# Kernel tuning notes

Measured on AMD Instinct MI355X. Metric: run time of the kernel, lower is better.

The kernel has to match this reference:

```python
import jax, jax.numpy as jnp
import numpy as np

IN_F, OUT_F, BLOCK, NBLK = 1024, 4096, 256, 16
TOPK = NBLK // 4  # 4, as in forward: n_blocks // 4


def setup_inputs() -> dict:
    key = jax.random.key(0)
    ks = jax.random.split(key, 7)
    s = 1.0 / np.sqrt(IN_F)
    s2 = 1.0 / np.sqrt(OUT_F)
    return {
        "x": jax.random.normal(ks[0], (4, 4096, IN_F), jnp.float32),
        "router_w": jax.random.uniform(ks[1], (NBLK, IN_F), jnp.float32, -s, s),
        "router_b": jax.random.uniform(ks[2], (NBLK,), jnp.float32, -s, s),
        "w1": jax.random.uniform(ks[3], (OUT_F, IN_F), jnp.float32, -s, s),
        "b1": jax.random.uniform(ks[4], (OUT_F,), jnp.float32, -s, s),
        "w2": jax.random.uniform(ks[5], (IN_F, OUT_F), jnp.float32, -s2, s2),
        "b2": jax.random.uniform(ks[6], (IN_F,), jnp.float32, -s2, s2),
    }


def reference(x, router_w, router_b, w1, b1, w2, b2):
    x_shape = x.shape
    xf = x.reshape(-1, IN_F)  # [N, d]
    n = xf.shape[0]
    # router: Linear + softmax, then top-k block selection per token
    prob = jax.nn.softmax(xf @ router_w.T + router_b, axis=-1)  # [N, n_blocks]
    _, idx = jax.lax.top_k(prob, TOPK)  # [N, k]
    mask = jnp.zeros((n, NBLK), bool).at[jnp.arange(n)[:, None], idx].set(True)
    # RoutedLinearRow: per-block fc1, zeros at unselected blocks
    w1b = w1.reshape(NBLK, BLOCK, IN_F)
    b1b = b1.reshape(NBLK, BLOCK)
    h = jnp.einsum('nd,ibd->nib', xf, w1b) + b1b  # [N, n_blocks, block]
    h = jnp.where(mask[:, :, None], h, jnp.zeros((), h.dtype))
    h = jax.nn.relu(h)
    # RoutedLinearCol: only selected blocks contribute
    w2b = w2.reshape(IN_F, NBLK, BLOCK)
    y = jnp.einsum('nib,dib->nd', jnp.where(mask[:, :, None], h, 0.0), w2b) + b2
    return y.reshape(x_shape)
```

## Files before the change

kernel.cpp:

```cpp
#include <hip/hip_runtime.h>
#include <hip/hip_bf16.h>

#define NTOK   16384
#define INF    1024
#define OUTF   4096
#define NBLK   16
#define BLKSZ  256
#define KTOP   4

typedef short bf16x8 __attribute__((ext_vector_type(8)));
typedef float f32x4 __attribute__((ext_vector_type(4)));
typedef unsigned short u16x8 __attribute__((ext_vector_type(8)));

__device__ __forceinline__ unsigned short f2bf(float f) {
  unsigned u = __float_as_uint(f);
  u += 0x7FFFu + ((u >> 16) & 1u);
  return (unsigned short)(u >> 16);
}

__device__ __forceinline__ void load_lds16(const void* g, void* l) {
  __builtin_amdgcn_global_load_lds(
      (const __attribute__((address_space(1))) unsigned int*)g,
      (__attribute__((address_space(3))) unsigned int*)l, 16, 0, 0);
}

__device__ __forceinline__ double shfl_xor_d(double v, int m) {
  long long l = __double_as_longlong(v);
  int lo = (int)(l & 0xFFFFFFFFll), hi = (int)(l >> 32);
  lo = __shfl_xor(lo, m);
  hi = __shfl_xor(hi, m);
  return __longlong_as_double(((long long)hi << 32) | (unsigned long long)(unsigned)lo);
}

__device__ __forceinline__ int pi_perm(int j) {
  return (j & 128) | ((j & 7) << 4) | ((j >> 3) & 15);
}

__global__ __launch_bounds__(256) void k_cvt_router(
    const float* __restrict__ x, const float* __restrict__ rw,
    const float* __restrict__ rb, const float* __restrict__ w1,
    const float* __restrict__ w2, const float* __restrict__ b1,
    unsigned* __restrict__ tok_blocks, unsigned* __restrict__ counts,
    unsigned short* __restrict__ xb, unsigned short* __restrict__ w1b,
    unsigned short* __restrict__ w2p, float* __restrict__ b1p) {
  __shared__ float4 rwl[4096];
  const int tid = threadIdx.x;
  const float4* rw4 = (const float4*)rw;
  for (int i = tid; i < 4096; i += 256) rwl[i] = rw4[i];
  __syncthreads();

  const int n = blockIdx.x * 32 + (tid >> 3);
  const int q = tid & 7;
  double p[16];
#pragma unroll
  for (int j = 0; j < 16; ++j) p[j] = 0.0;
  const float4* xr = (const float4*)(x + (size_t)n * INF);
  ushort4* xbr = (ushort4*)(xb + (size_t)n * INF);
#pragma unroll 4
  for (int i = 0; i < 32; ++i) {
    const int d4 = q + i * 8;
    const float4 xv = xr[d4];
    ushort4 o;
    o.x = f2bf(xv.x); o.y = f2bf(xv.y); o.z = f2bf(xv.z); o.w = f2bf(xv.w);
    xbr[d4] = o;
#pragma unroll
    for (int j = 0; j < 16; ++j) {
      const float4 wv = rwl[j * 256 + d4];
      p[j] = fma((double)xv.x, (double)wv.x, p[j]);
      p[j] = fma((double)xv.y, (double)wv.y, p[j]);
      p[j] = fma((double)xv.z, (double)wv.z, p[j]);
      p[j] = fma((double)xv.w, (double)wv.w, p[j]);
    }
  }
#pragma unroll
  for (int j = 0; j < 16; ++j) {
    double v = p[j];
    v += shfl_xor_d(v, 1);
    v += shfl_xor_d(v, 2);
    v += shfl_xor_d(v, 4);
    p[j] = v + (double)rb[j];
  }

  __syncthreads();
  unsigned* hist = (unsigned*)rwl;
  if (tid < 16) hist[tid] = 0;
  __syncthreads();

  if (q == 0) {
    unsigned packed = 0;
#pragma unroll
    for (int j = 0; j < 16; ++j) {
      int r = 0;
#pragma unroll
      for (int j2 = 0; j2 < 16; ++j2)
        r += (int)((p[j2] > p[j]) | ((p[j2] == p[j]) & (j2 < j)));
      if (r < KTOP) packed |= (unsigned)j << (8 * r);
    }
    tok_blocks[n] = packed;
    atomicAdd(&hist[packed & 15u], 1u);
    atomicAdd(&hist[(packed >> 8) & 15u], 1u);
    atomicAdd(&hist[(packed >> 16) & 15u], 1u);
    atomicAdd(&hist[(packed >> 24) & 15u], 1u);
  }
  __syncthreads();
  if (tid < 16 && hist[tid]) atomicAdd(&counts[tid], hist[tid]);

  const size_t stride = (size_t)gridDim.x * 256;
  for (size_t i = (size_t)blockIdx.x * 256 + tid; i < 1573376; i += stride) {
    if (i < 1048576) {
      float4 v = ((const float4*)w1)[i];
      ushort4 o;
      o.x = f2bf(v.x); o.y = f2bf(v.y); o.z = f2bf(v.z); o.w = f2bf(v.w);
      ((ushort4*)w1b)[i] = o;
    } else if (i < 1572864) {
      const size_t g = i - 1048576;
      const int d = (int)(g >> 9);
      const int rest = (int)(g & 511);
      const int jg = rest * 8;
      const int blk = jg >> 8;
      const int j0 = jg & 255;
      const float* src = w2 + (size_t)d * 4096 + blk * 256;
      u16x8 o;
#pragma unroll
      for (int ni = 0; ni < 8; ++ni) o[ni] = f2bf(src[pi_perm(j0 + ni)]);
      *(u16x8*)(w2p + (size_t)d * 4096 + jg) = o;
    } else {
      const int idx = (int)(i - 1572864);
      const int jg = idx * 8;
      const int blk = jg >> 8;
      const int j0 = jg & 255;
      const float* src = b1 + blk * 256;
      float o[8];
#pragma unroll
      for (int ni = 0; ni < 8; ++ni) o[ni] = src[pi_perm(j0 + ni)];
      float4* dst = (float4*)(b1p + jg);
      dst[0] = make_float4(o[0], o[1], o[2], o[3]);
      dst[1] = make_float4(o[4], o[5], o[6], o[7]);
    }
  }
}

__global__ __launch_bounds__(256) void k_build(
    const unsigned* __restrict__ tok_blocks, const unsigned* __restrict__ counts,
    unsigned* __restrict__ alloc, unsigned short* __restrict__ list) {
  unsigned offl[16];
  {
    unsigned o = 0;
#pragma unroll
    for (int i = 0; i < 16; ++i) { offl[i] = o; o += (counts[i] + 127u) & ~127u; }
  }
  const int n = blockIdx.x * 256 + threadIdx.x;
  const unsigned packed = tok_blocks[n];
  const int lane = threadIdx.x & 63;
#pragma unroll
  for (int b = 0; b < 16; ++b) {
    int r = -1;
#pragma unroll
    for (int q = 0; q < 4; ++q)
      if (((packed >> (8 * q)) & 15u) == (unsigned)b) r = q;
    unsigned long long m = __ballot(r >= 0);
    if (m) {
      int leader = __ffsll((unsigned long long)m) - 1;
      unsigned base = 0;
      if (lane == leader) base = offl[b] + atomicAdd(&alloc[b], (unsigned)__popcll(m));
      base = (unsigned)__shfl((int)base, leader);
      if (r >= 0) {
        unsigned pos = base + (unsigned)__popcll(m & ((1ull << lane) - 1ull));
        list[pos] = (unsigned short)(n | (r << 14));
      }
    }
  }
}

__global__ __launch_bounds__(256, 2) void k_ffn(
    const unsigned short* __restrict__ xb, const unsigned short* __restrict__ w1b,
    const unsigned short* __restrict__ w2p, const float* __restrict__ b1p,
    const unsigned short* __restrict__ list, const unsigned* __restrict__ counts,
    unsigned short* __restrict__ part) {
  __shared__ __align__(16) char lds[73728];
  char* const As0 = lds + 32768;
  char* const As1 = lds + 36864;
  char* const Bs0 = lds + 40960;
  char* const Bs1 = lds + 57344;

  const int bid0 = blockIdx.x;
  const int bid = (bid0 & 7) * 256 + (bid0 >> 3);
  const int blk = bid >> 7;
  const int tile = bid & 127;
  unsigned cnt = 0, goffBase = 0;
  {
    unsigned o = 0;
#pragma unroll
    for (int i = 0; i < 16; ++i) {
      const unsigned c = counts[i];
      if (i == blk) { cnt = c; goffBase = o; }
      o += (c + 127u) & ~127u;
    }
  }
  if ((unsigned)(tile * 64) >= cnt) return;
  const unsigned goff = goffBase + tile * 64;
  const int rem = (int)cnt - tile * 64;

  const int tid = threadIdx.x;
  const int lane = tid & 63;
  const int wid = tid >> 6;
  const int wr = wid >> 1;
  const int wc = wid & 1;
  const int c16 = lane & 15;
  const int kc = lane >> 4;

  const int srow = tid >> 2;
  const int schunk = tid & 3;
  const unsigned tokS = list[goff + srow] & 0x3FFFu;

#define STAGE_A(buf, k0)                                                        \
  load_lds16(xb + (size_t)tokS * INF + (k0) +                                   \
                 ((schunk ^ ((srow >> 1) & 3)) * 8),                            \
             (buf) + tid * 16);

#define STAGE_B1(buf, k0)                                                       \
  _Pragma("unroll")                                                             \
  for (int l = 0; l < 4; ++l) {                                                 \
    const int idx = l * 256 + tid;                                              \
    const int row = idx >> 2;                                                   \
    load_lds16(w1b + (size_t)(blk * 256 + row) * INF + (k0) +                   \
                   (((idx & 3) ^ ((row >> 1) & 3)) * 8),                        \
               (buf) + idx * 16);                                               \
  }

#define COMPUTE_A(abuf, bbuf)                                                   \
  {                                                                             \
    bf16x8 a[2], b[8];                                                          \
    _Pragma("unroll")                                                           \
    for (int mi = 0; mi < 2; ++mi) {                                            \
      const int row = wr * 32 + mi * 16 + c16;                                  \
      a[mi] = *(const bf16x8*)((abuf) + row * 64 +                              \
                               ((kc ^ ((row >> 1) & 3)) << 4));                 \
    }                                                                           \
    _Pragma("unroll")                                                           \
    for (int ni = 0; ni < 8; ++ni) {                                            \
      const int row = wc * 128 + ni * 16 + c16;                                 \
      b[ni] = *(const bf16x8*)((bbuf) + row * 64 +                              \
                               ((kc ^ ((row >> 1) & 3)) << 4));                 \
    }                                                                           \
    _Pragma("unroll")                                                           \
    for (int mi = 0; mi < 2; ++mi)                                              \
      _Pragma("unroll")                                                         \
      for (int ni = 0; ni < 8; ++ni)                                            \
        acc[mi][ni] =                                                           \
            __builtin_amdgcn_mfma_f32_16x16x32_bf16(a[mi], b[ni], acc[mi][ni], 0, 0, 0); \
  }

  f32x4 acc[2][8] = {};
  STAGE_A(As0, 0);
  STAGE_B1(Bs0, 0);
  __syncthreads();
#pragma unroll 1
  for (int kk = 0; kk < 16; ++kk) {
    const int k0 = kk * 64;
    STAGE_A(As1, k0 + 32);
    STAGE_B1(Bs1, k0 + 32);
    COMPUTE_A(As0, Bs0);
    __syncthreads();
    if (kk < 15) {
      STAGE_A(As0, k0 + 64);
      STAGE_B1(Bs0, k0 + 64);
    }
    COMPUTE_A(As1, Bs1);
    __syncthreads();
  }

#define STAGE_B2(buf, it)                                                       \
  {                                                                             \
    const int ns2 = (it) >> 3, k02 = ((it) & 7) * 32;                           \
    _Pragma("unroll")                                                           \
    for (int l = 0; l < 4; ++l) {                                               \
      const int idx = l * 256 + tid;                                            \
      const int row = idx >> 2;                                                 \
      load_lds16(w2p + (size_t)(ns2 * 256 + row) * OUTF + blk * 256 + k02 +     \
                     (((idx & 3) ^ ((row >> 1) & 3)) * 8),                      \
                 (buf) + idx * 16);                                             \
    }                                                                           \
  }

#define COMPUTE_B(bbuf, k02)                                                    \
  {                                                                             \
    bf16x8 a[2], b[8];                                                          \
    _Pragma("unroll")                                                           \
    for (int mi = 0; mi < 2; ++mi) {                                            \
      const int row = wr * 32 + mi * 16 + c16;                                  \
      const int co = ((k02) >> 3) + kc;                                         \
      a[mi] = *(const bf16x8*)(lds + row * 512 +                                \
                               (((co & ~7) | ((co & 7) ^ (row & 7))) << 4));    \
    }                                                                           \
    _Pragma("unroll")                                                           \
    for (int ni = 0; ni < 8; ++ni) {                                            \
      const int row = wc * 128 + ni * 16 + c16;                                 \
      b[ni] = *(const bf16x8*)((bbuf) + row * 64 +                              \
                               ((kc ^ ((row >> 1) & 3)) << 4));                 \
    }                                                                           \
    _Pragma("unroll")                                                           \
    for (int mi = 0; mi < 2; ++mi)                                              \
      _Pragma("unroll")                                                         \
      for (int ni = 0; ni < 8; ++ni)                                            \
        acc2[mi][ni] =                                                          \
            __builtin_amdgcn_mfma_f32_16x16x32_bf16(a[mi], b[ni], acc2[mi][ni], 0, 0, 0); \
  }

  STAGE_B2(Bs0, 0);

  {
    const float4* bp = (const float4*)(b1p + blk * 256 + wc * 128 + c16 * 8);
    const float4 bv0 = bp[0], bv1 = bp[1];
    const float bvv[8] = {bv0.x, bv0.y, bv0.z, bv0.w, bv1.x, bv1.y, bv1.z, bv1.w};
    const int chunk = wc * 16 + c16;
    const int cslot = (chunk & ~7);
    const int clow  = (chunk & 7);
#pragma unroll
    for (int mi = 0; mi < 2; ++mi) {
#pragma unroll
      for (int i = 0; i < 4; ++i) {
        const int row = wr * 32 + mi * 16 + (lane >> 4) * 4 + i;
        u16x8 wv;
#pragma unroll
        for (int ni = 0; ni < 8; ++ni) {
          float v = acc[mi][ni][i] + bvv[ni];
          v = v > 0.f ? v : 0.f;
          wv[ni] = f2bf(v);
        }
        *(u16x8*)(lds + row * 512 + ((cslot | (clow ^ (row & 7))) << 4)) = wv;
      }
    }
  }
  __syncthreads();

#pragma unroll 1
  for (int ns = 0; ns < 4; ++ns) {
    f32x4 acc2[2][8] = {};
#pragma unroll 1
    for (int jj = 0; jj < 4; ++jj) {
      const int it = ns * 8 + jj * 2;
      STAGE_B2(Bs1, it + 1);
      COMPUTE_B(Bs0, jj * 64);
      __syncthreads();
      if (it + 2 < 32) STAGE_B2(Bs0, it + 2);
      COMPUTE_B(Bs1, jj * 64 + 32);
      __syncthreads();
    }
#pragma unroll
    for (int mi = 0; mi < 2; ++mi) {
#pragma unroll
      for (int i = 0; i < 4; ++i) {
        const int row = wr * 32 + mi * 16 + (lane >> 4) * 4 + i;
        if (row < rem) {
          const unsigned e = list[goff + row];
          u16x8 wv;
#pragma unroll
          for (int ni = 0; ni < 8; ++ni) wv[ni] = f2bf(acc2[mi][ni][i]);
          *(u16x8*)(part + ((size_t)(e & 0x3FFFu) * 4 + (e >> 14)) * 1024 +
                    ns * 256 + wc * 128 + c16 * 8) = wv;
        }
      }
    }
  }
#undef STAGE_A
#undef STAGE_B1
#undef STAGE_B2
#undef COMPUTE_A
#undef COMPUTE_B
}

__global__ __launch_bounds__(256) void k_reduce(const unsigned short* __restrict__ part,
                                                const float* __restrict__ b2,
                                                float* __restrict__ out) {
  __shared__ float lds[8 * 1028];
  const int tid = threadIdx.x;
  const int tok0 = blockIdx.x * 8;
  const int tok_l = tid >> 5;
  const int l32 = tid & 31;
  const unsigned short* pbase = part + (size_t)(tok0 + tok_l) * 4096;

#pragma unroll
  for (int g = 0; g < 4; ++g) {
    const int idx = g * 32 + l32;
    const int p0 = idx * 8;
    float s[8] = {0.f, 0.f, 0.f, 0.f, 0.f, 0.f, 0.f, 0.f};
#pragma unroll
    for (int sl = 0; sl < 4; ++sl) {
      u16x8 v = *(const u16x8*)(pbase + sl * 1024 + p0);
#pragma unroll
      for (int j = 0; j < 8; ++j)
        s[j] += __uint_as_float((unsigned)(unsigned short)v[j] << 16);
    }
    const int ns = idx >> 5, wcb = (idx >> 4) & 1, cc = idx & 15;
#pragma unroll
    for (int ni = 0; ni < 8; ++ni)
      lds[tok_l * 1028 + ns * 256 + wcb * 128 + ni * 16 + cc] = s[ni];
  }
  __syncthreads();
  const float4 b2v = ((const float4*)b2)[tid];
#pragma unroll
  for (int r = 0; r < 8; ++r) {
    f32x4 lv = *(f32x4*)&lds[r * 1028 + tid * 4];
    float4 o = make_float4(lv[0] + b2v.x, lv[1] + b2v.y, lv[2] + b2v.z, lv[3] + b2v.w);
    *(float4*)(out + (size_t)(tok0 + r) * 1024 + tid * 4) = o;
  }
}

extern "C" void kernel_launch(void* const* d_in, const int* in_sizes, int n_in,
                              void* d_out, int out_size, void* d_ws, size_t ws_size,
                              hipStream_t stream) {
  const float* x  = (const float*)d_in[0];
  const float* rw = (const float*)d_in[1];
  const float* rb = (const float*)d_in[2];
  const float* w1 = (const float*)d_in[3];
  const float* b1 = (const float*)d_in[4];
  const float* w2 = (const float*)d_in[5];
  const float* b2 = (const float*)d_in[6];
  float* out = (float*)d_out;

  char* ws = (char*)d_ws;
  unsigned short* part = (unsigned short*)(ws);
  unsigned short* xb   = (unsigned short*)(ws + 134217728);
  unsigned short* w1b  = (unsigned short*)(ws + 167772160);
  unsigned short* w2p  = (unsigned short*)(ws + 176160768);
  unsigned* tokb       = (unsigned*)(ws + 184549376);
  unsigned short* list = (unsigned short*)(ws + 184614912);
  float* b1p           = (float*)(ws + 184750080);
  unsigned* counts     = (unsigned*)(ws + 184766464);
  unsigned* alloc      = (unsigned*)(ws + 184766528);

  hipMemsetAsync(ws + 184766464, 0, 128, stream);
  k_cvt_router<<<dim3(512), dim3(256), 0, stream>>>(x, rw, rb, w1, w2, b1, tokb,
                                                    counts, xb, w1b, w2p, b1p);
  k_build<<<dim3(64), dim3(256), 0, stream>>>(tokb, counts, alloc, list);
  k_ffn<<<dim3(2048), dim3(256), 0, stream>>>(xb, w1b, w2p, b1p, list, counts, part);
  k_reduce<<<dim3(2048), dim3(256), 0, stream>>>(part, b2, out);
}
```

Before: 287.1 us.

## Split FFN tile across 8 waves with narrower per-wave N slices

```diff
diff --git a/kernel.cpp b/kernel.cpp
--- a/kernel.cpp
+++ b/kernel.cpp
@@ -11,6 +11,7 @@
 typedef short bf16x8 __attribute__((ext_vector_type(8)));
 typedef float f32x4 __attribute__((ext_vector_type(4)));
 typedef unsigned short u16x8 __attribute__((ext_vector_type(8)));
+typedef unsigned short u16x4 __attribute__((ext_vector_type(4)));
 
 __device__ __forceinline__ unsigned short f2bf(float f) {
   unsigned u = __float_as_uint(f);
@@ -32,8 +33,8 @@
   return __longlong_as_double(((long long)hi << 32) | (unsigned long long)(unsigned)lo);
 }
 
-__device__ __forceinline__ int pi_perm(int j) {
-  return (j & 128) | ((j & 7) << 4) | ((j >> 3) & 15);
+__device__ __forceinline__ int pi2(int j) {
+  return (j & 192) | ((j & 3) << 4) | ((j >> 2) & 15);
 }
 
 __global__ __launch_bounds__(256) void k_cvt_router(
@@ -122,7 +123,7 @@
       const float* src = w2 + (size_t)d * 4096 + blk * 256;
       u16x8 o;
 #pragma unroll
-      for (int ni = 0; ni < 8; ++ni) o[ni] = f2bf(src[pi_perm(j0 + ni)]);
+      for (int ni = 0; ni < 8; ++ni) o[ni] = f2bf(src[pi2(j0 + ni)]);
       *(u16x8*)(w2p + (size_t)d * 4096 + jg) = o;
     } else {
       const int idx = (int)(i - 1572864);
@@ -132,7 +133,7 @@
       const float* src = b1 + blk * 256;
       float o[8];
 #pragma unroll
-      for (int ni = 0; ni < 8; ++ni) o[ni] = src[pi_perm(j0 + ni)];
+      for (int ni = 0; ni < 8; ++ni) o[ni] = src[pi2(j0 + ni)];
       float4* dst = (float4*)(b1p + jg);
       dst[0] = make_float4(o[0], o[1], o[2], o[3]);
       dst[1] = make_float4(o[4], o[5], o[6], o[7]);
@@ -172,7 +173,7 @@
   }
 }
 
-__global__ __launch_bounds__(256, 2) void k_ffn(
+__global__ __launch_bounds__(512, 4) void k_ffn(
     const unsigned short* __restrict__ xb, const unsigned short* __restrict__ w1b,
     const unsigned short* __restrict__ w2p, const float* __restrict__ b1p,
     const unsigned short* __restrict__ list, const unsigned* __restrict__ counts,
@@ -204,24 +205,25 @@
   const int tid = threadIdx.x;
   const int lane = tid & 63;
   const int wid = tid >> 6;
-  const int wr = wid >> 1;
-  const int wc = wid & 1;
+  const int wr = wid >> 2;
+  const int wc = wid & 3;
   const int c16 = lane & 15;
-  const int kc = lane >> 4;
+  const int kc4 = lane >> 4;
 
   const int srow = tid >> 2;
   const int schunk = tid & 3;
-  const unsigned tokS = list[goff + srow] & 0x3FFFu;
+  const unsigned tokS = list[goff + (srow & 63)] & 0x3FFFu;
 
 #define STAGE_A(buf, k0)                                                        \
-  load_lds16(xb + (size_t)tokS * INF + (k0) +                                   \
-                 ((schunk ^ ((srow >> 1) & 3)) * 8),                            \
-             (buf) + tid * 16);
+  if (tid < 256)                                                                \
+    load_lds16(xb + (size_t)tokS * INF + (k0) +                                 \
+                   ((schunk ^ ((srow >> 1) & 3)) * 8),                          \
+               (buf) + tid * 16);
 
 #define STAGE_B1(buf, k0)                                                       \
   _Pragma("unroll")                                                             \
-  for (int l = 0; l < 4; ++l) {                                                 \
-    const int idx = l * 256 + tid;                                              \
+  for (int l = 0; l < 2; ++l) {                                                 \
+    const int idx = l * 512 + tid;                                              \
     const int row = idx >> 2;                                                   \
     load_lds16(w1b + (size_t)(blk * 256 + row) * INF + (k0) +                   \
                    (((idx & 3) ^ ((row >> 1) & 3)) * 8),                        \
@@ -230,28 +232,28 @@
 
 #define COMPUTE_A(abuf, bbuf)                                                   \
   {                                                                             \
-    bf16x8 a[2], b[8];                                                          \
+    bf16x8 a[2], b[4];                                                          \
     _Pragma("unroll")                                                           \
     for (int mi = 0; mi < 2; ++mi) {                                            \
       const int row = wr * 32 + mi * 16 + c16;                                  \
       a[mi] = *(const bf16x8*)((abuf) + row * 64 +                              \
-                               ((kc ^ ((row >> 1) & 3)) << 4));                 \
+                               ((kc4 ^ ((row >> 1) & 3)) << 4));                \
     }                                                                           \
     _Pragma("unroll")                                                           \
-    for (int ni = 0; ni < 8; ++ni) {                                            \
-      const int row = wc * 128 + ni * 16 + c16;                                 \
+    for (int ni = 0; ni < 4; ++ni) {                                            \
+      const int row = wc * 64 + ni * 16 + c16;                                  \
       b[ni] = *(const bf16x8*)((bbuf) + row * 64 +                              \
-                               ((kc ^ ((row >> 1) & 3)) << 4));                 \
+                               ((kc4 ^ ((row >> 1) & 3)) << 4));                \
     }                                                                           \
     _Pragma("unroll")                                                           \
     for (int mi = 0; mi < 2; ++mi)                                              \
       _Pragma("unroll")                                                         \
-      for (int ni = 0; ni < 8; ++ni)                                            \
+      for (int ni = 0; ni < 4; ++ni)                                            \
         acc[mi][ni] =                                                           \
             __builtin_amdgcn_mfma_f32_16x16x32_bf16(a[mi], b[ni], acc[mi][ni], 0, 0, 0); \
   }
 
-  f32x4 acc[2][8] = {};
+  f32x4 acc[2][4] = {};
   STAGE_A(As0, 0);
   STAGE_B1(Bs0, 0);
   __syncthreads();
@@ -274,8 +276,8 @@
   {                                                                             \
     const int ns2 = (it) >> 3, k02 = ((it) & 7) * 32;                           \
     _Pragma("unroll")                                                           \
-    for (int l = 0; l < 4; ++l) {                                               \
-      const int idx = l * 256 + tid;                                            \
+    for (int l = 0; l < 2; ++l) {                                               \
+      const int idx = l * 512 + tid;                                            \
       const int row = idx >> 2;                                                 \
       load_lds16(w2p + (size_t)(ns2 * 256 + row) * OUTF + blk * 256 + k02 +     \
                      (((idx & 3) ^ ((row >> 1) & 3)) * 8),                      \
@@ -285,24 +287,24 @@
 
 #define COMPUTE_B(bbuf, k02)                                                    \
   {                                                                             \
-    bf16x8 a[2], b[8];                                                          \
+    bf16x8 a[2], b[4];                                                          \
     _Pragma("unroll")                                                           \
     for (int mi = 0; mi < 2; ++mi) {                                            \
       const int row = wr * 32 + mi * 16 + c16;                                  \
-      const int co = ((k02) >> 3) + kc;                                         \
+      const int co = ((k02) >> 3) + kc4;                                        \
       a[mi] = *(const bf16x8*)(lds + row * 512 +                                \
                                (((co & ~7) | ((co & 7) ^ (row & 7))) << 4));    \
     }                                                                           \
     _Pragma("unroll")                                                           \
-    for (int ni = 0; ni < 8; ++ni) {                                            \
-      const int row = wc * 128 + ni * 16 + c16;                                 \
+    for (int ni = 0; ni < 4; ++ni) {                                            \
+      const int row = wc * 64 + ni * 16 + c16;                                  \
       b[ni] = *(const bf16x8*)((bbuf) + row * 64 +                              \
-                               ((kc ^ ((row >> 1) & 3)) << 4));                 \
+                               ((kc4 ^ ((row >> 1) & 3)) << 4));                \
     }                                                                           \
     _Pragma("unroll")                                                           \
     for (int mi = 0; mi < 2; ++mi)                                              \
       _Pragma("unroll")                                                         \
-      for (int ni = 0; ni < 8; ++ni)                                            \
+      for (int ni = 0; ni < 4; ++ni)                                            \
         acc2[mi][ni] =                                                          \
             __builtin_amdgcn_mfma_f32_16x16x32_bf16(a[mi], b[ni], acc2[mi][ni], 0, 0, 0); \
   }
@@ -310,25 +312,22 @@
   STAGE_B2(Bs0, 0);
 
   {
-    const float4* bp = (const float4*)(b1p + blk * 256 + wc * 128 + c16 * 8);
-    const float4 bv0 = bp[0], bv1 = bp[1];
-    const float bvv[8] = {bv0.x, bv0.y, bv0.z, bv0.w, bv1.x, bv1.y, bv1.z, bv1.w};
-    const int chunk = wc * 16 + c16;
-    const int cslot = (chunk & ~7);
-    const int clow  = (chunk & 7);
+    const float4 bv = *(const float4*)(b1p + blk * 256 + wc * 64 + c16 * 4);
+    const float bvv[4] = {bv.x, bv.y, bv.z, bv.w};
 #pragma unroll
     for (int mi = 0; mi < 2; ++mi) {
 #pragma unroll
       for (int i = 0; i < 4; ++i) {
         const int row = wr * 32 + mi * 16 + (lane >> 4) * 4 + i;
-        u16x8 wv;
-#pragma unroll
-        for (int ni = 0; ni < 8; ++ni) {
+        u16x4 wv;
+#pragma unroll
+        for (int ni = 0; ni < 4; ++ni) {
           float v = acc[mi][ni][i] + bvv[ni];
           v = v > 0.f ? v : 0.f;
           wv[ni] = f2bf(v);
         }
-        *(u16x8*)(lds + row * 512 + ((cslot | (clow ^ (row & 7))) << 4)) = wv;
+        *(u16x4*)(lds + row * 512 +
+                  ((wc * 8 + ((c16 >> 1) ^ (row & 7))) << 4) + (c16 & 1) * 8) = wv;
       }
     }
   }
@@ -336,7 +335,7 @@
 
 #pragma unroll 1
   for (int ns = 0; ns < 4; ++ns) {
-    f32x4 acc2[2][8] = {};
+    f32x4 acc2[2][4] = {};
 #pragma unroll 1
     for (int jj = 0; jj < 4; ++jj) {
       const int it = ns * 8 + jj * 2;
@@ -354,11 +353,11 @@
         const int row = wr * 32 + mi * 16 + (lane >> 4) * 4 + i;
         if (row < rem) {
           const unsigned e = list[goff + row];
-          u16x8 wv;
-#pragma unroll
-          for (int ni = 0; ni < 8; ++ni) wv[ni] = f2bf(acc2[mi][ni][i]);
-          *(u16x8*)(part + ((size_t)(e & 0x3FFFu) * 4 + (e >> 14)) * 1024 +
-                    ns * 256 + wc * 128 + c16 * 8) = wv;
+          u16x4 wv;
+#pragma unroll
+          for (int ni = 0; ni < 4; ++ni) wv[ni] = f2bf(acc2[mi][ni][i]);
+          *(u16x4*)(part + ((size_t)(e & 0x3FFFu) * 4 + (e >> 14)) * 1024 +
+                    ns * 256 + wc * 64 + c16 * 4) = wv;
         }
       }
     }
@@ -381,8 +380,8 @@
   const unsigned short* pbase = part + (size_t)(tok0 + tok_l) * 4096;
 
 #pragma unroll
-  for (int g = 0; g < 4; ++g) {
-    const int idx = g * 32 + l32;
+  for (int g4 = 0; g4 < 4; ++g4) {
+    const int idx = g4 * 32 + l32;
     const int p0 = idx * 8;
     float s[8] = {0.f, 0.f, 0.f, 0.f, 0.f, 0.f, 0.f, 0.f};
 #pragma unroll
@@ -392,10 +391,13 @@
       for (int j = 0; j < 8; ++j)
         s[j] += __uint_as_float((unsigned)(unsigned short)v[j] << 16);
     }
-    const int ns = idx >> 5, wcb = (idx >> 4) & 1, cc = idx & 15;
-#pragma unroll
-    for (int ni = 0; ni < 8; ++ni)
-      lds[tok_l * 1028 + ns * 256 + wcb * 128 + ni * 16 + cc] = s[ni];
+    const int g = idx >> 5, r = idx & 31;
+    const int wcb = r >> 3, c16b = (r & 7) * 2;
+#pragma unroll
+    for (int j = 0; j < 8; ++j) {
+      const int ni = j & 3, cc = c16b + (j >> 2);
+      lds[tok_l * 1028 + g * 256 + wcb * 64 + ni * 16 + cc] = s[j];
+    }
   }
   __syncthreads();
   const float4 b2v = ((const float4*)b2)[tid];
@@ -434,6 +436,6 @@
   k_cvt_router<<<dim3(512), dim3(256), 0, stream>>>(x, rw, rb, w1, w2, b1, tokb,
                                                     counts, xb, w1b, w2p, b1p);
   k_build<<<dim3(64), dim3(256), 0, stream>>>(tokb, counts, alloc, list);
-  k_ffn<<<dim3(2048), dim3(256), 0, stream>>>(xb, w1b, w2p, b1p, list, counts, part);
+  k_ffn<<<dim3(2048), dim3(512), 0, stream>>>(xb, w1b, w2p, b1p, list, counts, part);
   k_reduce<<<dim3(2048), dim3(256), 0, stream>>>(part, b2, out);
 }
```

Measured after the change: 277.2 us. 3.4% less time.
